# Performance work log

Measured on AMD Instinct MI355X. Metric: run time of the kernel, lower is better.

## Reference

```python
import jax, jax.numpy as jnp
import numpy as np

K = 4          # neighbors
R = 2          # step_ratio
OUT = 64       # output_size

def knn_idx(x, k):
    # x: (B, C, N) -> indices of k nearest neighbors (incl. self): (B, N, k)
    xx = jnp.sum(x * x, axis=1)                       # (B, N)
    inner = jnp.einsum('bcn,bcm->bnm', x, x)          # (B, N, N)
    neg_dist = 2.0 * inner - xx[:, :, None] - xx[:, None, :]
    _, idx = jax.lax.top_k(neg_dist, k)               # largest neg_dist = nearest
    return idx

def setup_inputs() -> dict:
    key = jax.random.key(0)
    ks = jax.random.split(key, 7)
    B, C, N = 16, 64, 2048
    s = 0.05
    return {
        'x':  jax.random.normal(ks[0], (B, C, N), jnp.float32),
        'w1': jax.random.normal(ks[1], (OUT, 2 * C), jnp.float32) * s,
        'b1': jax.random.normal(ks[2], (OUT,), jnp.float32) * s,
        'w2': jax.random.normal(ks[3], (OUT * R, 2 * C + OUT), jnp.float32) * s,
        'b2': jax.random.normal(ks[4], (OUT * R,), jnp.float32) * s,
        'w3': jax.random.normal(ks[5], (OUT, OUT), jnp.float32) * s,
        'b3': jax.random.normal(ks[6], (OUT,), jnp.float32) * s,
    }

def reference(x, w1, b1, w2, b2, w3, b3):
    B, C, N = x.shape
    idx = knn_idx(x, K)                                # (B, N, K)
    xt = jnp.transpose(x, (0, 2, 1))                   # (B, N, C)
    neighbors = xt[jnp.arange(B)[:, None, None], idx]  # (B, N, K, C)
    center = jnp.broadcast_to(xt[:, :, None, :], neighbors.shape)
    feat = jnp.concatenate([center, neighbors], axis=-1)   # (B, N, K, 2C), minus_center=False
    # get_graph_feature returns (B, 2C, N, K); module permutes to (B, 2C, K, N)
    f = jnp.transpose(feat, (0, 3, 2, 1))              # (B, 2C, K, N)
    e1 = jnp.einsum('oc,bckn->bokn', w1, f) + b1[None, :, None, None]
    e = jax.nn.relu(jnp.concatenate([e1, f], axis=1))  # (B, 2C+OUT, K, N)
    e2 = jax.nn.relu(jnp.einsum('oc,bckn->bokn', w2, e) + b2[None, :, None, None])  # (B, OUT*R, K, N)
    # permute(0,2,3,1) -> (B,K,N,OUT*R), view -> (B,K,N*R,OUT), permute -> (B,OUT,K,N*R)
    e2 = jnp.transpose(e2, (0, 2, 3, 1)).reshape(B, K, N * R, OUT)
    e2 = jnp.transpose(e2, (0, 3, 1, 2))               # (B, OUT, K, N*R)
    e3 = jnp.einsum('oc,bckn->bokn', w3, e2) + b3[None, :, None, None]
    return jnp.max(e3, axis=2)                          # (B, OUT, N*R)
```

## Files before the change

### kernel.cpp

```cpp
#include <hip/hip_runtime.h>
#include <hip/hip_bf16.h>

#define BB 16
#define CC 64
#define NN 2048
#define KK 4
#define NPART 4
#define JPER (NN / NPART)
#define NCAND 32
#define RSTRIDE 80

typedef unsigned short u16;
typedef unsigned int u32;
typedef __attribute__((ext_vector_type(4))) float f32x4;
typedef __attribute__((ext_vector_type(16))) float f32x16;
typedef __attribute__((ext_vector_type(8))) short short8;

__device__ __forceinline__ float bf2f(u16 u) {
    unsigned int x = ((unsigned int)u) << 16;
    float f;
    __builtin_memcpy(&f, &x, 4);
    return f;
}
__device__ __forceinline__ u16 f2bf(float f) {
    __hip_bfloat16 h = __float2bfloat16(f);
    u16 u;
    __builtin_memcpy(&u, &h, 2);
    return u;
}
__device__ __forceinline__ unsigned int pk2(float a, float b) {
    return (unsigned int)f2bf(a) | ((unsigned int)f2bf(b) << 16);
}
__device__ __forceinline__ u32 umx(u32 a, u32 b) { return a > b ? a : b; }
__device__ __forceinline__ u32 umn(u32 a, u32 b) { return a < b ? a : b; }

__global__ __launch_bounds__(256) void k_prep(const float* __restrict__ x,
                                              float* __restrict__ xt,
                                              double* __restrict__ xx64,
                                              u16* __restrict__ xpk,
                                              const float* __restrict__ w1,
                                              const float* __restrict__ w2,
                                              const float* __restrict__ w3,
                                              u16* __restrict__ wb1,
                                              u16* __restrict__ wb2,
                                              u16* __restrict__ wb3) {
    int b = blockIdx.y;
    int n = blockIdx.x * 256 + threadIdx.x;

    {
        int t = (blockIdx.y * gridDim.x + blockIdx.x) * 256 + threadIdx.x;
        int stride = gridDim.x * gridDim.y * 256;
        for (int idx = t; idx < 64 * 128; idx += stride) {
            int o = idx >> 7, k = idx & 127;
            int cb = o >> 4, lr = o & 15, ks = k >> 5, g = (k >> 3) & 3, e = k & 7;
            wb1[((cb * 4 + ks) * 64 + g * 16 + lr) * 8 + e] = f2bf(w1[idx]);
        }
        for (int idx = t; idx < 128 * 192; idx += stride) {
            int o = idx / 192, k = idx - o * 192;
            int cb = o >> 4, lr = o & 15, ks = k >> 5, g = (k >> 3) & 3, e = k & 7;
            wb2[((cb * 6 + ks) * 64 + g * 16 + lr) * 8 + e] = f2bf(w2[idx]);
        }
        for (int idx = t; idx < 64 * 64; idx += stride) {
            int o = idx >> 6, k = idx & 63;
            int cb = o >> 4, lr = o & 15, ks = k >> 5, g = (k >> 3) & 3, e = k & 7;
            wb3[((cb * 2 + ks) * 64 + g * 16 + lr) * 8 + e] = f2bf(w3[idx]);
        }
    }

    const float* xb = x + (size_t)b * CC * NN;
    float v[CC];
    float s = 0.f;
    double s64 = 0.0;
#pragma unroll
    for (int c = 0; c < CC; c++) {
        v[c] = xb[(size_t)c * NN + n];
        s = fmaf(v[c], v[c], s);
        s64 += (double)v[c] * (double)v[c];
    }
    float4* dst = (float4*)(xt + ((size_t)b * NN + n) * CC);
#pragma unroll
    for (int q = 0; q < 16; q++) {
        dst[q] = make_float4(v[4 * q], v[4 * q + 1], v[4 * q + 2], v[4 * q + 3]);
    }
    xx64[b * NN + n] = s64;
    u16* dp = xpk + ((size_t)b * NN + n) * RSTRIDE;
#pragma unroll
    for (int q = 0; q < 8; q++) {
        uint4 u;
        u.x = pk2(v[8 * q], v[8 * q + 1]);
        u.y = pk2(v[8 * q + 2], v[8 * q + 3]);
        u.z = pk2(v[8 * q + 4], v[8 * q + 5]);
        u.w = pk2(v[8 * q + 6], v[8 * q + 7]);
        *(uint4*)(dp + q * 8) = u;
    }
    u16 hi = f2bf(s);
    u16 lo = f2bf(s - bf2f(hi));
    uint4 u8;
    u8.x = (unsigned int)hi | ((unsigned int)lo << 16);
    u8.y = 0x00003F80u;
    u8.z = 0; u8.w = 0;
    *(uint4*)(dp + 64) = u8;
    uint4 z = {0, 0, 0, 0};
    *(uint4*)(dp + 72) = z;
}

__global__ __launch_bounds__(256) void k_knn3(const u16* __restrict__ xpk,
                                              u16* __restrict__ cand) {
    int tid = threadIdx.x;
    int lin = blockIdx.x;
    int swz = (lin & 7) * 128 + (lin >> 3);
    int ib = swz & 15;
    int part = (swz >> 4) & 3;
    int b = swz >> 6;
    int i0 = ib * 128;
    int j00 = part * JPER;

    __shared__ u16 Bb[2 * 2 * 10 * 32 * 8];

    int w = tid >> 6, l = tid & 63;
    int lc = l & 31, lh = l >> 5;
    int hb4 = lh * 4;

    short8 ifrag[5];
    {
        const u16* ip = xpk + ((size_t)b * NN + i0 + w * 32 + lc) * RSTRIDE + lh * 8;
#pragma unroll
        for (int ks = 0; ks < 4; ks++) ifrag[ks] = *(const short8*)(ip + ks * 16);
        short8 f4 = {0, 0, 0, 0, 0, 0, 0, 0};
        if (lh == 0) {
            f4[0] = (short)0xBF00;
            f4[1] = (short)0xBF00;
            f4[2] = (short)0x4300;
        }
        ifrag[4] = f4;
    }

    u32 v0 = 0, v1 = 0, v2 = 0, v3 = 0;

#define CE(a, b) { u32 mx_ = umx(a, b); b = umn(a, b); a = mx_; }

#define STAGE(rr, bf)                                                              \
    {                                                                              \
        int jb = j00 + (rr) * 64;                                                  \
        for (int g = tid; g < 640; g += 256) {                                     \
            int rw = g / 10, c = g - rw * 10;                                      \
            uint4 u = *(const uint4*)(xpk + ((size_t)b * NN + jb + rw) * RSTRIDE + \
                                      c * 8);                                      \
            int sub = rw >> 5, r32 = rw & 31;                                      \
            *(uint4*)((char*)Bb + (bf) * 10240 + sub * 5120 + c * 512 +            \
                      ((r32 ^ (c & 7)) * 16)) = u;                                 \
        }                                                                          \
    }

    STAGE(0, 0);

    for (int r = 0; r < JPER / 64; r++) {
        __syncthreads();
        if (r + 1 < JPER / 64) STAGE(r + 1, (r + 1) & 1);

        const char* bufp = (const char*)Bb + (r & 1) * 10240;
        f32x16 acc0, acc1;
#pragma unroll
        for (int e = 0; e < 16; e++) {
            acc0[e] = 0.f;
            acc1[e] = 0.f;
        }
#pragma unroll
        for (int ks = 0; ks < 5; ks++) {
            int c = ks * 2 + lh;
            int boff = c * 512 + ((lc ^ (c & 7)) * 16);
            short8 a0 = *(const short8*)(bufp + boff);
            short8 a1 = *(const short8*)(bufp + 5120 + boff);
            acc0 = __builtin_amdgcn_mfma_f32_32x32x16_bf16(a0, ifrag[ks], acc0, 0, 0, 0);
            acc1 = __builtin_amdgcn_mfma_f32_32x32x16_bf16(a1, ifrag[ks], acc1, 0, 0, 0);
        }
#pragma unroll
        for (int sub = 0; sub < 2; sub++) {
            const f32x16& acc = sub ? acc1 : acc0;
            int jlb = r * 64 + sub * 32 + hb4;
            u32 kk[16];
#pragma unroll
            for (int rg = 0; rg < 16; rg++) {
                u32 u;
                float f = acc[rg];
                __builtin_memcpy(&u, &f, 4);
                int coff = (rg & 3) + 8 * (rg >> 2);
                kk[rg] = (u & ~0x1FFu) | (u32)(jlb + coff);
            }
#pragma unroll
            for (int q = 0; q < 4; q++) {
                int p = q * 4;
                CE(kk[p + 0], kk[p + 2]); CE(kk[p + 1], kk[p + 3]);
                CE(kk[p + 0], kk[p + 1]); CE(kk[p + 2], kk[p + 3]);
                CE(kk[p + 1], kk[p + 2]);
            }
            kk[0] = umx(kk[0], kk[7]); kk[1] = umx(kk[1], kk[6]);
            kk[2] = umx(kk[2], kk[5]); kk[3] = umx(kk[3], kk[4]);
            CE(kk[0], kk[2]); CE(kk[1], kk[3]); CE(kk[0], kk[1]); CE(kk[2], kk[3]);
            kk[8] = umx(kk[8], kk[15]); kk[9] = umx(kk[9], kk[14]);
            kk[10] = umx(kk[10], kk[13]); kk[11] = umx(kk[11], kk[12]);
            CE(kk[8], kk[10]); CE(kk[9], kk[11]); CE(kk[8], kk[9]); CE(kk[10], kk[11]);
            kk[0] = umx(kk[0], kk[11]); kk[1] = umx(kk[1], kk[10]);
            kk[2] = umx(kk[2], kk[9]); kk[3] = umx(kk[3], kk[8]);
            CE(kk[0], kk[2]); CE(kk[1], kk[3]); CE(kk[0], kk[1]); CE(kk[2], kk[3]);
            v0 = umx(v0, kk[3]); v1 = umx(v1, kk[2]);
            v2 = umx(v2, kk[1]); v3 = umx(v3, kk[0]);
            CE(v0, v2); CE(v1, v3); CE(v0, v1); CE(v2, v3);
        }
    }
#undef STAGE
#undef CE

    size_t cb = ((size_t)b * NN + i0 + w * 32 + lc) * NCAND + part * 8 + lh * 4;
    cand[cb + 0] = (u16)(j00 + (v0 & 0x1FF));
    cand[cb + 1] = (u16)(j00 + (v1 & 0x1FF));
    cand[cb + 2] = (u16)(j00 + (v2 & 0x1FF));
    cand[cb + 3] = (u16)(j00 + (v3 & 0x1FF));
}

__global__ __launch_bounds__(256) void k_knn_merge(const float* __restrict__ xt,
                                                   const double* __restrict__ xx64,
                                                   const u16* __restrict__ cand,
                                                   int* __restrict__ nidx) {
    __shared__ double sv[16 * 33];
    __shared__ double sxx[16 * 33];
    __shared__ u16 jc[16 * 33];

    int tid = threadIdx.x;
    int g = tid >> 4;
    int q = tid & 15;
    int nwg8 = (int)(gridDim.x >> 3);
    int swz = (blockIdx.x & 7) * nwg8 + (blockIdx.x >> 3);
    size_t gp0 = (size_t)swz * 16;
    size_t bbase = (gp0 >> 11) << 11;

    for (int idx = tid; idx < 16 * 32; idx += 256) {
        int p = idx >> 5, c = idx & 31;
        u16 j = cand[(gp0 + p) * NCAND + c];
        jc[p * 33 + c] = j;
        sxx[p * 33 + c] = xx64[bbase + j];
    }
    __syncthreads();

    float4 a = ((const float4*)(xt + (gp0 + g) * CC))[q];

    float4 bv[NCAND];
#pragma unroll
    for (int c = 0; c < NCAND; c++) {
        bv[c] = ((const float4*)(xt + (bbase + jc[g * 33 + c]) * CC))[q];
    }

#pragma unroll
    for (int c0 = 0; c0 < NCAND; c0 += 4) {
        double d0 = (double)a.x * bv[c0 + 0].x + (double)a.y * bv[c0 + 0].y +
                    (double)a.z * bv[c0 + 0].z + (double)a.w * bv[c0 + 0].w;
        double d1 = (double)a.x * bv[c0 + 1].x + (double)a.y * bv[c0 + 1].y +
                    (double)a.z * bv[c0 + 1].z + (double)a.w * bv[c0 + 1].w;
        double d2 = (double)a.x * bv[c0 + 2].x + (double)a.y * bv[c0 + 2].y +
                    (double)a.z * bv[c0 + 2].z + (double)a.w * bv[c0 + 2].w;
        double d3 = (double)a.x * bv[c0 + 3].x + (double)a.y * bv[c0 + 3].y +
                    (double)a.z * bv[c0 + 3].z + (double)a.w * bv[c0 + 3].w;
        d0 += __shfl_xor(d0, 8); d1 += __shfl_xor(d1, 8);
        d2 += __shfl_xor(d2, 8); d3 += __shfl_xor(d3, 8);
        d0 += __shfl_xor(d0, 4); d1 += __shfl_xor(d1, 4);
        d2 += __shfl_xor(d2, 4); d3 += __shfl_xor(d3, 4);
        d0 += __shfl_xor(d0, 2); d1 += __shfl_xor(d1, 2);
        d2 += __shfl_xor(d2, 2); d3 += __shfl_xor(d3, 2);
        d0 += __shfl_xor(d0, 1); d1 += __shfl_xor(d1, 1);
        d2 += __shfl_xor(d2, 1); d3 += __shfl_xor(d3, 1);
        if (q == 0) {
            sv[g * 33 + c0 + 0] = 2.0 * d0 - sxx[g * 33 + c0 + 0];
            sv[g * 33 + c0 + 1] = 2.0 * d1 - sxx[g * 33 + c0 + 1];
            sv[g * 33 + c0 + 2] = 2.0 * d2 - sxx[g * 33 + c0 + 2];
            sv[g * 33 + c0 + 3] = 2.0 * d3 - sxx[g * 33 + c0 + 3];
        }
    }
    __syncthreads();

    if (tid < 16) {
        int p = tid;
        double v4[4];
        int id4[4];
#pragma unroll
        for (int s = 0; s < 4; s++) {
            v4[s] = -1e300;
            id4[s] = 0x7fffffff;
        }
        for (int cc = 0; cc < NCAND; cc++) {
            double cv = sv[p * 33 + cc];
            int ci = jc[p * 33 + cc];
#pragma unroll
            for (int s = 0; s < 4; s++) {
                bool take = (cv > v4[s]) || (cv == v4[s] && ci < id4[s]);
                double nv = take ? cv : v4[s];
                int ni = take ? ci : id4[s];
                double ov = take ? v4[s] : cv;
                int oi = take ? id4[s] : ci;
                v4[s] = nv;
                id4[s] = ni;
                cv = ov;
                ci = oi;
            }
        }
        size_t gp2 = gp0 + p;
#pragma unroll
        for (int s = 0; s < 4; s++) nidx[gp2 * 4 + s] = id4[s];
    }
}

__global__ __launch_bounds__(256) void k_mlp(const u16* __restrict__ xpk,
                                             const int* __restrict__ nidx,
                                             const u16* __restrict__ wb1,
                                             const u16* __restrict__ wb2,
                                             const u16* __restrict__ wb3,
                                             const float* __restrict__ b1,
                                             const float* __restrict__ b2,
                                             const float* __restrict__ b3,
                                             float* __restrict__ out) {
    int nch = blockIdx.x;
    int b = blockIdx.y;
    int n0 = nch * 16;
    int tid = threadIdx.x;

    __shared__ u16 Fb[64 * 128];
    __shared__ u16 E1b[64 * 64];
    __shared__ u16 E2b[64 * 128];
    __shared__ float Ob[64 * 36];
    __shared__ int ji[64];

    if (tid < 64) ji[tid] = nidx[((size_t)b * NN + n0) * KK + tid];
    __syncthreads();

    for (int g = tid; g < 64 * 16; g += 256) {
        int it = g >> 4, q = g & 15;
        int half = q >> 3, cq = q & 7;
        int srcn = half ? ji[it] : (n0 + (it >> 2));
        uint4 u = *(const uint4*)(xpk + ((size_t)b * NN + srcn) * RSTRIDE + cq * 8);
        int byte = (it * 256 + half * 128 + cq * 16) ^ ((it & 7) << 4);
        *(uint4*)((char*)Fb + byte) = u;
    }
    __syncthreads();

    int w = tid >> 6, l = tid & 63;
    int lr = l & 15, lg = l >> 4;

    {
        f32x4 acc[4];
#pragma unroll
        for (int g = 0; g < 4; g++) acc[g] = (f32x4){0.f, 0.f, 0.f, 0.f};
#pragma unroll
        for (int ks = 0; ks < 4; ks++) {
            short8 bw = *(const short8*)(wb1 + ((size_t)(w * 4 + ks) * 64 + l) * 8);
#pragma unroll
            for (int g = 0; g < 4; g++) {
                int arow = g * 16 + lr;
                int off = (arow * 256 + ks * 64 + lg * 16) ^ ((arow & 7) << 4);
                short8 a = *(const short8*)((const char*)Fb + off);
                acc[g] = __builtin_amdgcn_mfma_f32_16x16x32_bf16(a, bw, acc[g], 0, 0, 0);
            }
        }
        float bias = b1[w * 16 + lr];
#pragma unroll
        for (int g = 0; g < 4; g++) {
#pragma unroll
            for (int q = 0; q < 4; q++) {
                int item = g * 16 + lg * 4 + q;
                float vv = fmaxf(acc[g][q] + bias, 0.f);
                int byte = (item * 128 + (w * 16 + lr) * 2) ^ ((item & 7) << 4);
                *(u16*)((char*)E1b + byte) = f2bf(vv);
            }
        }
    }
    __syncthreads();

    {
        f32x4 acc[4][2];
#pragma unroll
        for (int g = 0; g < 4; g++)
#pragma unroll
            for (int c2 = 0; c2 < 2; c2++) acc[g][c2] = (f32x4){0.f, 0.f, 0.f, 0.f};
#pragma unroll
        for (int ks = 0; ks < 6; ks++) {
            short8 bw0 = *(const short8*)(wb2 + ((size_t)((w * 2) * 6 + ks) * 64 + l) * 8);
            short8 bw1 = *(const short8*)(wb2 + ((size_t)((w * 2 + 1) * 6 + ks) * 64 + l) * 8);
#pragma unroll
            for (int g = 0; g < 4; g++) {
                int arow = g * 16 + lr;
                int aswz = (arow & 7) << 4;
                short8 a;
                if (ks < 2) {
                    int off = (arow * 128 + ks * 64 + lg * 16) ^ aswz;
                    a = *(const short8*)((const char*)E1b + off);
                } else {
                    int off = (arow * 256 + (ks - 2) * 64 + lg * 16) ^ aswz;
                    uint4 u = *(const uint4*)((const char*)Fb + off);
                    unsigned int m;
                    m = ((u.x >> 15) & 0x10001u) * 0xFFFFu; u.x &= ~m;
                    m = ((u.y >> 15) & 0x10001u) * 0xFFFFu; u.y &= ~m;
                    m = ((u.z >> 15) & 0x10001u) * 0xFFFFu; u.z &= ~m;
                    m = ((u.w >> 15) & 0x10001u) * 0xFFFFu; u.w &= ~m;
                    __builtin_memcpy(&a, &u, 16);
                }
                acc[g][0] = __builtin_amdgcn_mfma_f32_16x16x32_bf16(a, bw0, acc[g][0], 0, 0, 0);
                acc[g][1] = __builtin_amdgcn_mfma_f32_16x16x32_bf16(a, bw1, acc[g][1], 0, 0, 0);
            }
        }
#pragma unroll
        for (int c2 = 0; c2 < 2; c2++) {
            float bias = b2[(w * 2 + c2) * 16 + lr];
#pragma unroll
            for (int g = 0; g < 4; g++) {
#pragma unroll
                for (int q = 0; q < 4; q++) {
                    int item = g * 16 + lg * 4 + q;
                    float vv = fmaxf(acc[g][c2][q] + bias, 0.f);
                    int byte = (item * 256 + ((w * 2 + c2) * 16 + lr) * 2) ^ ((item & 7) << 4);
                    *(u16*)((char*)E2b + byte) = f2bf(vv);
                }
            }
        }
    }
    __syncthreads();

    {
        f32x4 acc[4][2];
#pragma unroll
        for (int g = 0; g < 4; g++)
#pragma unroll
            for (int r = 0; r < 2; r++) acc[g][r] = (f32x4){0.f, 0.f, 0.f, 0.f};
#pragma unroll
        for (int ks = 0; ks < 2; ks++) {
            short8 bw = *(const short8*)(wb3 + ((size_t)(w * 2 + ks) * 64 + l) * 8);
#pragma unroll
            for (int g = 0; g < 4; g++) {
                int arow = g * 16 + lr;
                int aswz = (arow & 7) << 4;
#pragma unroll
                for (int r = 0; r < 2; r++) {
                    int off = (arow * 256 + r * 128 + ks * 64 + lg * 16) ^ aswz;
                    short8 a = *(const short8*)((const char*)E2b + off);
                    acc[g][r] = __builtin_amdgcn_mfma_f32_16x16x32_bf16(a, bw, acc[g][r], 0, 0, 0);
                }
            }
        }
        float bias = b3[w * 16 + lr];
        int o = w * 16 + lr;
#pragma unroll
        for (int g = 0; g < 4; g++) {
            int nl = g * 4 + lg;
#pragma unroll
            for (int r = 0; r < 2; r++) {
                float m = fmaxf(fmaxf(acc[g][r][0], acc[g][r][1]),
                                fmaxf(acc[g][r][2], acc[g][r][3])) + bias;
                Ob[o * 36 + nl * 2 + r] = m;
            }
        }
    }
    __syncthreads();

    {
        int o = tid >> 2, q = tid & 3;
        float4 v0 = *(const float4*)&Ob[o * 36 + q * 8];
        float4 v1 = *(const float4*)&Ob[o * 36 + q * 8 + 4];
        float* dst = out + ((size_t)(b * 64 + o)) * 4096 + n0 * 2 + q * 8;
        ((float4*)dst)[0] = v0;
        ((float4*)dst)[1] = v1;
    }
}

extern "C" void kernel_launch(void* const* d_in, const int* in_sizes, int n_in,
                              void* d_out, int out_size, void* d_ws, size_t ws_size,
                              hipStream_t stream) {
    const float* x = (const float*)d_in[0];
    const float* w1 = (const float*)d_in[1];
    const float* b1 = (const float*)d_in[2];
    const float* w2 = (const float*)d_in[3];
    const float* b2 = (const float*)d_in[4];
    const float* w3 = (const float*)d_in[5];
    const float* b3 = (const float*)d_in[6];
    float* out = (float*)d_out;

    float* xt = (float*)d_ws;
    u16* xpk = (u16*)(xt + (size_t)BB * NN * CC);
    double* xx64 = (double*)(xpk + (size_t)BB * NN * RSTRIDE);
    int* nidx = (int*)(xx64 + (size_t)BB * NN);
    u16* cand = (u16*)(nidx + (size_t)BB * NN * KK);
    u16* wb1 = cand + (size_t)BB * NN * NCAND;
    u16* wb2 = wb1 + 64 * 128;
    u16* wb3 = wb2 + 128 * 192;

    k_prep<<<dim3(NN / 256, BB), 256, 0, stream>>>(x, xt, xx64, xpk,
                                                   w1, w2, w3, wb1, wb2, wb3);
    k_knn3<<<dim3(NN / 128 * NPART * BB), 256, 0, stream>>>(xpk, cand);
    k_knn_merge<<<dim3(BB * NN / 16), 256, 0, stream>>>(xt, xx64, cand, nidx);
    k_mlp<<<dim3(NN / 16, BB), 256, 0, stream>>>(xpk, nidx, wb1, wb2, wb3, b1, b2, b3, out);
}
```

Before: 107.4 us.

## Fuse knn, merge and MLP kernels into one persistent kernel with grid barriers

Replaces three separate launches (candidate kNN, merge, MLP) with a single persistent kernel of 768 blocks. The blocks loop over work units for each phase and separate the phases with a spin-on-atomic grid barrier. The barrier counter is reset in the prep kernel. This removes inter-kernel launch gaps and tail effects. In exchange it relies on all 768 blocks being co-resident (launch_bounds 256,3 with about 50KB of shared memory), otherwise the barrier can deadlock or time out. It also adds the cost of atomic spinning.

```diff
diff --git a/kernel.cpp b/kernel.cpp
--- a/kernel.cpp
+++ b/kernel.cpp
@@ -9,6 +9,7 @@
 #define JPER (NN / NPART)
 #define NCAND 32
 #define RSTRIDE 80
+#define GRID_F 768
 
 typedef unsigned short u16;
 typedef unsigned int u32;
@@ -43,7 +44,9 @@
                                               const float* __restrict__ w3,
                                               u16* __restrict__ wb1,
                                               u16* __restrict__ wb2,
-                                              u16* __restrict__ wb3) {
+                                              u16* __restrict__ wb3,
+                                              u32* __restrict__ bar) {
+    if (blockIdx.x == 0 && blockIdx.y == 0 && threadIdx.x < 2) bar[threadIdx.x] = 0;
     int b = blockIdx.y;
     int n = blockIdx.x * 256 + threadIdx.x;
 
@@ -104,367 +107,386 @@
     *(uint4*)(dp + 72) = z;
 }
 
-__global__ __launch_bounds__(256) void k_knn3(const u16* __restrict__ xpk,
-                                              u16* __restrict__ cand) {
+__device__ __forceinline__ void grid_bar(u32* cnt, u32 target) {
+    __syncthreads();
+    if (threadIdx.x == 0) {
+        __threadfence();
+        atomicAdd(cnt, 1u);
+        int it = 0;
+        while (atomicAdd(cnt, 0u) < target && it < 100000000) it++;
+        __threadfence();
+    }
+    __syncthreads();
+}
+
+__global__ __launch_bounds__(256, 3) void k_fused(const float* __restrict__ xt,
+                                                  const double* __restrict__ xx64,
+                                                  const u16* __restrict__ xpk,
+                                                  u16* __restrict__ cand,
+                                                  int* __restrict__ nidx,
+                                                  const u16* __restrict__ wb1,
+                                                  const u16* __restrict__ wb2,
+                                                  const u16* __restrict__ wb3,
+                                                  const float* __restrict__ b1,
+                                                  const float* __restrict__ b2,
+                                                  const float* __restrict__ b3,
+                                                  float* __restrict__ out,
+                                                  u32* __restrict__ bar) {
+    __shared__ __align__(16) char smem[50432];
     int tid = threadIdx.x;
     int lin = blockIdx.x;
-    int swz = (lin & 7) * 128 + (lin >> 3);
-    int ib = swz & 15;
-    int part = (swz >> 4) & 3;
-    int b = swz >> 6;
-    int i0 = ib * 128;
-    int j00 = part * JPER;
-
-    __shared__ u16 Bb[2 * 2 * 10 * 32 * 8];
-
-    int w = tid >> 6, l = tid & 63;
-    int lc = l & 31, lh = l >> 5;
-    int hb4 = lh * 4;
-
-    short8 ifrag[5];
-    {
-        const u16* ip = xpk + ((size_t)b * NN + i0 + w * 32 + lc) * RSTRIDE + lh * 8;
-#pragma unroll
-        for (int ks = 0; ks < 4; ks++) ifrag[ks] = *(const short8*)(ip + ks * 16);
-        short8 f4 = {0, 0, 0, 0, 0, 0, 0, 0};
-        if (lh == 0) {
-            f4[0] = (short)0xBF00;
-            f4[1] = (short)0xBF00;
-            f4[2] = (short)0x4300;
-        }
-        ifrag[4] = f4;
-    }
-
-    u32 v0 = 0, v1 = 0, v2 = 0, v3 = 0;
+
+    for (int u = lin; u < 1024; u += GRID_F) {
+        __syncthreads();
+        int swz = (u & 7) * 128 + (u >> 3);
+        int ib = swz & 15;
+        int part = (swz >> 4) & 3;
+        int b = swz >> 6;
+        int i0 = ib * 128;
+        int j00 = part * JPER;
+        u16* Bb = (u16*)smem;
+
+        int w = tid >> 6, l = tid & 63;
+        int lc = l & 31, lh = l >> 5;
+        int hb4 = lh * 4;
+
+        short8 ifrag[5];
+        {
+            const u16* ip = xpk + ((size_t)b * NN + i0 + w * 32 + lc) * RSTRIDE + lh * 8;
+#pragma unroll
+            for (int ks = 0; ks < 4; ks++) ifrag[ks] = *(const short8*)(ip + ks * 16);
+            short8 f4 = {0, 0, 0, 0, 0, 0, 0, 0};
+            if (lh == 0) {
+                f4[0] = (short)0xBF00;
+                f4[1] = (short)0xBF00;
+                f4[2] = (short)0x4300;
+            }
+            ifrag[4] = f4;
+        }
+
+        u32 v0 = 0, v1 = 0, v2 = 0, v3 = 0;
 
 #define CE(a, b) { u32 mx_ = umx(a, b); b = umn(a, b); a = mx_; }
-
 #define STAGE(rr, bf)                                                              \
     {                                                                              \
         int jb = j00 + (rr) * 64;                                                  \
         for (int g = tid; g < 640; g += 256) {                                     \
             int rw = g / 10, c = g - rw * 10;                                      \
-            uint4 u = *(const uint4*)(xpk + ((size_t)b * NN + jb + rw) * RSTRIDE + \
+            uint4 uu = *(const uint4*)(xpk + ((size_t)b * NN + jb + rw) * RSTRIDE +\
                                       c * 8);                                      \
             int sub = rw >> 5, r32 = rw & 31;                                      \
             *(uint4*)((char*)Bb + (bf) * 10240 + sub * 5120 + c * 512 +            \
-                      ((r32 ^ (c & 7)) * 16)) = u;                                 \
+                      ((r32 ^ (c & 7)) * 16)) = uu;                                \
         }                                                                          \
     }
 
-    STAGE(0, 0);
-
-    for (int r = 0; r < JPER / 64; r++) {
-        __syncthreads();
-        if (r + 1 < JPER / 64) STAGE(r + 1, (r + 1) & 1);
-
-        const char* bufp = (const char*)Bb + (r & 1) * 10240;
-        f32x16 acc0, acc1;
-#pragma unroll
-        for (int e = 0; e < 16; e++) {
-            acc0[e] = 0.f;
-            acc1[e] = 0.f;
-        }
-#pragma unroll
-        for (int ks = 0; ks < 5; ks++) {
-            int c = ks * 2 + lh;
-            int boff = c * 512 + ((lc ^ (c & 7)) * 16);
-            short8 a0 = *(const short8*)(bufp + boff);
-            short8 a1 = *(const short8*)(bufp + 5120 + boff);
-            acc0 = __builtin_amdgcn_mfma_f32_32x32x16_bf16(a0, ifrag[ks], acc0, 0, 0, 0);
-            acc1 = __builtin_amdgcn_mfma_f32_32x32x16_bf16(a1, ifrag[ks], acc1, 0, 0, 0);
-        }
-#pragma unroll
-        for (int sub = 0; sub < 2; sub++) {
-            const f32x16& acc = sub ? acc1 : acc0;
-            int jlb = r * 64 + sub * 32 + hb4;
-            u32 kk[16];
-#pragma unroll
-            for (int rg = 0; rg < 16; rg++) {
-                u32 u;
-                float f = acc[rg];
-                __builtin_memcpy(&u, &f, 4);
-                int coff = (rg & 3) + 8 * (rg >> 2);
-                kk[rg] = (u & ~0x1FFu) | (u32)(jlb + coff);
-            }
-#pragma unroll
-            for (int q = 0; q < 4; q++) {
-                int p = q * 4;
-                CE(kk[p + 0], kk[p + 2]); CE(kk[p + 1], kk[p + 3]);
-                CE(kk[p + 0], kk[p + 1]); CE(kk[p + 2], kk[p + 3]);
-                CE(kk[p + 1], kk[p + 2]);
-            }
-            kk[0] = umx(kk[0], kk[7]); kk[1] = umx(kk[1], kk[6]);
-            kk[2] = umx(kk[2], kk[5]); kk[3] = umx(kk[3], kk[4]);
-            CE(kk[0], kk[2]); CE(kk[1], kk[3]); CE(kk[0], kk[1]); CE(kk[2], kk[3]);
-            kk[8] = umx(kk[8], kk[15]); kk[9] = umx(kk[9], kk[14]);
-            kk[10] = umx(kk[10], kk[13]); kk[11] = umx(kk[11], kk[12]);
-            CE(kk[8], kk[10]); CE(kk[9], kk[11]); CE(kk[8], kk[9]); CE(kk[10], kk[11]);
-            kk[0] = umx(kk[0], kk[11]); kk[1] = umx(kk[1], kk[10]);
-            kk[2] = umx(kk[2], kk[9]); kk[3] = umx(kk[3], kk[8]);
-            CE(kk[0], kk[2]); CE(kk[1], kk[3]); CE(kk[0], kk[1]); CE(kk[2], kk[3]);
-            v0 = umx(v0, kk[3]); v1 = umx(v1, kk[2]);
-            v2 = umx(v2, kk[1]); v3 = umx(v3, kk[0]);
-            CE(v0, v2); CE(v1, v3); CE(v0, v1); CE(v2, v3);
-        }
-    }
+        STAGE(0, 0);
+
+        for (int r = 0; r < JPER / 64; r++) {
+            __syncthreads();
+            if (r + 1 < JPER / 64) STAGE(r + 1, (r + 1) & 1);
+
+            const char* bufp = (const char*)Bb + (r & 1) * 10240;
+            f32x16 acc0, acc1;
+#pragma unroll
+            for (int e = 0; e < 16; e++) {
+                acc0[e] = 0.f;
+                acc1[e] = 0.f;
+            }
+#pragma unroll
+            for (int ks = 0; ks < 5; ks++) {
+                int c = ks * 2 + lh;
+                int boff = c * 512 + ((lc ^ (c & 7)) * 16);
+                short8 a0 = *(const short8*)(bufp + boff);
+                short8 a1 = *(const short8*)(bufp + 5120 + boff);
+                acc0 = __builtin_amdgcn_mfma_f32_32x32x16_bf16(a0, ifrag[ks], acc0, 0, 0, 0);
+                acc1 = __builtin_amdgcn_mfma_f32_32x32x16_bf16(a1, ifrag[ks], acc1, 0, 0, 0);
+            }
+#pragma unroll
+            for (int sub = 0; sub < 2; sub++) {
+                const f32x16& acc = sub ? acc1 : acc0;
+                int jlb = r * 64 + sub * 32 + hb4;
+                u32 kk[16];
+#pragma unroll
+                for (int rg = 0; rg < 16; rg++) {
+                    u32 uu;
+                    float f = acc[rg];
+                    __builtin_memcpy(&uu, &f, 4);
+                    int coff = (rg & 3) + 8 * (rg >> 2);
+                    kk[rg] = (uu & ~0x1FFu) | (u32)(jlb + coff);
+                }
+#pragma unroll
+                for (int q = 0; q < 4; q++) {
+                    int p = q * 4;
+                    CE(kk[p + 0], kk[p + 2]); CE(kk[p + 1], kk[p + 3]);
+                    CE(kk[p + 0], kk[p + 1]); CE(kk[p + 2], kk[p + 3]);
+                    CE(kk[p + 1], kk[p + 2]);
+                }
+                kk[0] = umx(kk[0], kk[7]); kk[1] = umx(kk[1], kk[6]);
+                kk[2] = umx(kk[2], kk[5]); kk[3] = umx(kk[3], kk[4]);
+                CE(kk[0], kk[2]); CE(kk[1], kk[3]); CE(kk[0], kk[1]); CE(kk[2], kk[3]);
+                kk[8] = umx(kk[8], kk[15]); kk[9] = umx(kk[9], kk[14]);
+                kk[10] = umx(kk[10], kk[13]); kk[11] = umx(kk[11], kk[12]);
+                CE(kk[8], kk[10]); CE(kk[9], kk[11]); CE(kk[8], kk[9]); CE(kk[10], kk[11]);
+                kk[0] = umx(kk[0], kk[11]); kk[1] = umx(kk[1], kk[10]);
+                kk[2] = umx(kk[2], kk[9]); kk[3] = umx(kk[3], kk[8]);
+                CE(kk[0], kk[2]); CE(kk[1], kk[3]); CE(kk[0], kk[1]); CE(kk[2], kk[3]);
+                v0 = umx(v0, kk[3]); v1 = umx(v1, kk[2]);
+                v2 = umx(v2, kk[1]); v3 = umx(v3, kk[0]);
+                CE(v0, v2); CE(v1, v3); CE(v0, v1); CE(v2, v3);
+            }
+        }
 #undef STAGE
 #undef CE
 
-    size_t cb = ((size_t)b * NN + i0 + w * 32 + lc) * NCAND + part * 8 + lh * 4;
-    cand[cb + 0] = (u16)(j00 + (v0 & 0x1FF));
-    cand[cb + 1] = (u16)(j00 + (v1 & 0x1FF));
-    cand[cb + 2] = (u16)(j00 + (v2 & 0x1FF));
-    cand[cb + 3] = (u16)(j00 + (v3 & 0x1FF));
-}
-
-__global__ __launch_bounds__(256) void k_knn_merge(const float* __restrict__ xt,
-                                                   const double* __restrict__ xx64,
-                                                   const u16* __restrict__ cand,
-                                                   int* __restrict__ nidx) {
-    __shared__ double sv[16 * 33];
-    __shared__ double sxx[16 * 33];
-    __shared__ u16 jc[16 * 33];
-
-    int tid = threadIdx.x;
-    int g = tid >> 4;
-    int q = tid & 15;
-    int nwg8 = (int)(gridDim.x >> 3);
-    int swz = (blockIdx.x & 7) * nwg8 + (blockIdx.x >> 3);
-    size_t gp0 = (size_t)swz * 16;
-    size_t bbase = (gp0 >> 11) << 11;
-
-    for (int idx = tid; idx < 16 * 32; idx += 256) {
-        int p = idx >> 5, c = idx & 31;
-        u16 j = cand[(gp0 + p) * NCAND + c];
-        jc[p * 33 + c] = j;
-        sxx[p * 33 + c] = xx64[bbase + j];
-    }
-    __syncthreads();
-
-    float4 a = ((const float4*)(xt + (gp0 + g) * CC))[q];
-
-    float4 bv[NCAND];
-#pragma unroll
-    for (int c = 0; c < NCAND; c++) {
-        bv[c] = ((const float4*)(xt + (bbase + jc[g * 33 + c]) * CC))[q];
-    }
-
-#pragma unroll
-    for (int c0 = 0; c0 < NCAND; c0 += 4) {
-        double d0 = (double)a.x * bv[c0 + 0].x + (double)a.y * bv[c0 + 0].y +
-                    (double)a.z * bv[c0 + 0].z + (double)a.w * bv[c0 + 0].w;
-        double d1 = (double)a.x * bv[c0 + 1].x + (double)a.y * bv[c0 + 1].y +
-                    (double)a.z * bv[c0 + 1].z + (double)a.w * bv[c0 + 1].w;
-        double d2 = (double)a.x * bv[c0 + 2].x + (double)a.y * bv[c0 + 2].y +
-                    (double)a.z * bv[c0 + 2].z + (double)a.w * bv[c0 + 2].w;
-        double d3 = (double)a.x * bv[c0 + 3].x + (double)a.y * bv[c0 + 3].y +
-                    (double)a.z * bv[c0 + 3].z + (double)a.w * bv[c0 + 3].w;
-        d0 += __shfl_xor(d0, 8); d1 += __shfl_xor(d1, 8);
-        d2 += __shfl_xor(d2, 8); d3 += __shfl_xor(d3, 8);
-        d0 += __shfl_xor(d0, 4); d1 += __shfl_xor(d1, 4);
-        d2 += __shfl_xor(d2, 4); d3 += __shfl_xor(d3, 4);
-        d0 += __shfl_xor(d0, 2); d1 += __shfl_xor(d1, 2);
-        d2 += __shfl_xor(d2, 2); d3 += __shfl_xor(d3, 2);
-        d0 += __shfl_xor(d0, 1); d1 += __shfl_xor(d1, 1);
-        d2 += __shfl_xor(d2, 1); d3 += __shfl_xor(d3, 1);
-        if (q == 0) {
-            sv[g * 33 + c0 + 0] = 2.0 * d0 - sxx[g * 33 + c0 + 0];
-            sv[g * 33 + c0 + 1] = 2.0 * d1 - sxx[g * 33 + c0 + 1];
-            sv[g * 33 + c0 + 2] = 2.0 * d2 - sxx[g * 33 + c0 + 2];
-            sv[g * 33 + c0 + 3] = 2.0 * d3 - sxx[g * 33 + c0 + 3];
-        }
-    }
-    __syncthreads();
-
-    if (tid < 16) {
-        int p = tid;
-        double v4[4];
-        int id4[4];
-#pragma unroll
-        for (int s = 0; s < 4; s++) {
-            v4[s] = -1e300;
-            id4[s] = 0x7fffffff;
-        }
-        for (int cc = 0; cc < NCAND; cc++) {
-            double cv = sv[p * 33 + cc];
-            int ci = jc[p * 33 + cc];
+        size_t cb = ((size_t)b * NN + i0 + w * 32 + lc) * NCAND + part * 8 + lh * 4;
+        cand[cb + 0] = (u16)(j00 + (v0 & 0x1FF));
+        cand[cb + 1] = (u16)(j00 + (v1 & 0x1FF));
+        cand[cb + 2] = (u16)(j00 + (v2 & 0x1FF));
+        cand[cb + 3] = (u16)(j00 + (v3 & 0x1FF));
+    }
+
+    grid_bar(&bar[0], GRID_F);
+
+    for (int u = lin; u < 2048; u += GRID_F) {
+        __syncthreads();
+        double* sv = (double*)smem;
+        double* sxx = (double*)(smem + 4224);
+        u16* jc = (u16*)(smem + 8448);
+
+        int g = tid >> 4;
+        int q = tid & 15;
+        int swz = (u & 7) * 256 + (u >> 3);
+        size_t gp0 = (size_t)swz * 16;
+        size_t bbase = (gp0 >> 11) << 11;
+
+        for (int idx = tid; idx < 16 * 32; idx += 256) {
+            int p = idx >> 5, c = idx & 31;
+            u16 j = cand[(gp0 + p) * NCAND + c];
+            jc[p * 33 + c] = j;
+            sxx[p * 33 + c] = xx64[bbase + j];
+        }
+        __syncthreads();
+
+        float4 a = ((const float4*)(xt + (gp0 + g) * CC))[q];
+
+        float4 bv[NCAND];
+#pragma unroll
+        for (int c = 0; c < NCAND; c++) {
+            bv[c] = ((const float4*)(xt + (bbase + jc[g * 33 + c]) * CC))[q];
+        }
+
+#pragma unroll
+        for (int c0 = 0; c0 < NCAND; c0 += 4) {
+            double d0 = (double)a.x * bv[c0 + 0].x + (double)a.y * bv[c0 + 0].y +
+                        (double)a.z * bv[c0 + 0].z + (double)a.w * bv[c0 + 0].w;
+            double d1 = (double)a.x * bv[c0 + 1].x + (double)a.y * bv[c0 + 1].y +
+                        (double)a.z * bv[c0 + 1].z + (double)a.w * bv[c0 + 1].w;
+            double d2 = (double)a.x * bv[c0 + 2].x + (double)a.y * bv[c0 + 2].y +
+                        (double)a.z * bv[c0 + 2].z + (double)a.w * bv[c0 + 2].w;
+            double d3 = (double)a.x * bv[c0 + 3].x + (double)a.y * bv[c0 + 3].y +
+                        (double)a.z * bv[c0 + 3].z + (double)a.w * bv[c0 + 3].w;
+            d0 += __shfl_xor(d0, 8); d1 += __shfl_xor(d1, 8);
+            d2 += __shfl_xor(d2, 8); d3 += __shfl_xor(d3, 8);
+            d0 += __shfl_xor(d0, 4); d1 += __shfl_xor(d1, 4);
+            d2 += __shfl_xor(d2, 4); d3 += __shfl_xor(d3, 4);
+            d0 += __shfl_xor(d0, 2); d1 += __shfl_xor(d1, 2);
+            d2 += __shfl_xor(d2, 2); d3 += __shfl_xor(d3, 2);
+            d0 += __shfl_xor(d0, 1); d1 += __shfl_xor(d1, 1);
+            d2 += __shfl_xor(d2, 1); d3 += __shfl_xor(d3, 1);
+            if (q == 0) {
+                sv[g * 33 + c0 + 0] = 2.0 * d0 - sxx[g * 33 + c0 + 0];
+                sv[g * 33 + c0 + 1] = 2.0 * d1 - sxx[g * 33 + c0 + 1];
+                sv[g * 33 + c0 + 2] = 2.0 * d2 - sxx[g * 33 + c0 + 2];
+                sv[g * 33 + c0 + 3] = 2.0 * d3 - sxx[g * 33 + c0 + 3];
+            }
+        }
+        __syncthreads();
+
+        if (tid < 16) {
+            int p = tid;
+            double v4[4];
+            int id4[4];
 #pragma unroll
             for (int s = 0; s < 4; s++) {
-                bool take = (cv > v4[s]) || (cv == v4[s] && ci < id4[s]);
-                double nv = take ? cv : v4[s];
-                int ni = take ? ci : id4[s];
-                double ov = take ? v4[s] : cv;
-                int oi = take ? id4[s] : ci;
-                v4[s] = nv;
-                id4[s] = ni;
-                cv = ov;
-                ci = oi;
-            }
-        }
-        size_t gp2 = gp0 + p;
-#pragma unroll
-        for (int s = 0; s < 4; s++) nidx[gp2 * 4 + s] = id4[s];
-    }
-}
-
-__global__ __launch_bounds__(256) void k_mlp(const u16* __restrict__ xpk,
-                                             const int* __restrict__ nidx,
-                                             const u16* __restrict__ wb1,
-                                             const u16* __restrict__ wb2,
-                                             const u16* __restrict__ wb3,
-                                             const float* __restrict__ b1,
-                                             const float* __restrict__ b2,
-                                             const float* __restrict__ b3,
-                                             float* __restrict__ out) {
-    int nch = blockIdx.x;
-    int b = blockIdx.y;
-    int n0 = nch * 16;
-    int tid = threadIdx.x;
-
-    __shared__ u16 Fb[64 * 128];
-    __shared__ u16 E1b[64 * 64];
-    __shared__ u16 E2b[64 * 128];
-    __shared__ float Ob[64 * 36];
-    __shared__ int ji[64];
-
-    if (tid < 64) ji[tid] = nidx[((size_t)b * NN + n0) * KK + tid];
-    __syncthreads();
-
-    for (int g = tid; g < 64 * 16; g += 256) {
-        int it = g >> 4, q = g & 15;
-        int half = q >> 3, cq = q & 7;
-        int srcn = half ? ji[it] : (n0 + (it >> 2));
-        uint4 u = *(const uint4*)(xpk + ((size_t)b * NN + srcn) * RSTRIDE + cq * 8);
-        int byte = (it * 256 + half * 128 + cq * 16) ^ ((it & 7) << 4);
-        *(uint4*)((char*)Fb + byte) = u;
-    }
-    __syncthreads();
-
-    int w = tid >> 6, l = tid & 63;
-    int lr = l & 15, lg = l >> 4;
-
-    {
-        f32x4 acc[4];
-#pragma unroll
-        for (int g = 0; g < 4; g++) acc[g] = (f32x4){0.f, 0.f, 0.f, 0.f};
-#pragma unroll
-        for (int ks = 0; ks < 4; ks++) {
-            short8 bw = *(const short8*)(wb1 + ((size_t)(w * 4 + ks) * 64 + l) * 8);
-#pragma unroll
-            for (int g = 0; g < 4; g++) {
-                int arow = g * 16 + lr;
-                int off = (arow * 256 + ks * 64 + lg * 16) ^ ((arow & 7) << 4);
-                short8 a = *(const short8*)((const char*)Fb + off);
-                acc[g] = __builtin_amdgcn_mfma_f32_16x16x32_bf16(a, bw, acc[g], 0, 0, 0);
-            }
-        }
-        float bias = b1[w * 16 + lr];
-#pragma unroll
-        for (int g = 0; g < 4; g++) {
-#pragma unroll
-            for (int q = 0; q < 4; q++) {
-                int item = g * 16 + lg * 4 + q;
-                float vv = fmaxf(acc[g][q] + bias, 0.f);
-                int byte = (item * 128 + (w * 16 + lr) * 2) ^ ((item & 7) << 4);
-                *(u16*)((char*)E1b + byte) = f2bf(vv);
-            }
-        }
-    }
-    __syncthreads();
-
-    {
-        f32x4 acc[4][2];
-#pragma unroll
-        for (int g = 0; g < 4; g++)
-#pragma unroll
-            for (int c2 = 0; c2 < 2; c2++) acc[g][c2] = (f32x4){0.f, 0.f, 0.f, 0.f};
-#pragma unroll
-        for (int ks = 0; ks < 6; ks++) {
-            short8 bw0 = *(const short8*)(wb2 + ((size_t)((w * 2) * 6 + ks) * 64 + l) * 8);
-            short8 bw1 = *(const short8*)(wb2 + ((size_t)((w * 2 + 1) * 6 + ks) * 64 + l) * 8);
-#pragma unroll
-            for (int g = 0; g < 4; g++) {
-                int arow = g * 16 + lr;
-                int aswz = (arow & 7) << 4;
-                short8 a;
-                if (ks < 2) {
-                    int off = (arow * 128 + ks * 64 + lg * 16) ^ aswz;
-                    a = *(const short8*)((const char*)E1b + off);
-                } else {
-                    int off = (arow * 256 + (ks - 2) * 64 + lg * 16) ^ aswz;
-                    uint4 u = *(const uint4*)((const char*)Fb + off);
-                    unsigned int m;
-                    m = ((u.x >> 15) & 0x10001u) * 0xFFFFu; u.x &= ~m;
-                    m = ((u.y >> 15) & 0x10001u) * 0xFFFFu; u.y &= ~m;
-                    m = ((u.z >> 15) & 0x10001u) * 0xFFFFu; u.z &= ~m;
-                    m = ((u.w >> 15) & 0x10001u) * 0xFFFFu; u.w &= ~m;
-                    __builtin_memcpy(&a, &u, 16);
-                }
-                acc[g][0] = __builtin_amdgcn_mfma_f32_16x16x32_bf16(a, bw0, acc[g][0], 0, 0, 0);
-                acc[g][1] = __builtin_amdgcn_mfma_f32_16x16x32_bf16(a, bw1, acc[g][1], 0, 0, 0);
-            }
-        }
-#pragma unroll
-        for (int c2 = 0; c2 < 2; c2++) {
-            float bias = b2[(w * 2 + c2) * 16 + lr];
+                v4[s] = -1e300;
+                id4[s] = 0x7fffffff;
+            }
+            for (int cc = 0; cc < NCAND; cc++) {
+                double cv = sv[p * 33 + cc];
+                int ci = jc[p * 33 + cc];
+#pragma unroll
+                for (int s = 0; s < 4; s++) {
+                    bool take = (cv > v4[s]) || (cv == v4[s] && ci < id4[s]);
+                    double nv = take ? cv : v4[s];
+                    int ni = take ? ci : id4[s];
+                    double ov = take ? v4[s] : cv;
+                    int oi = take ? id4[s] : ci;
+                    v4[s] = nv;
+                    id4[s] = ni;
+                    cv = ov;
+                    ci = oi;
+                }
+            }
+            size_t gp2 = gp0 + p;
+#pragma unroll
+            for (int s = 0; s < 4; s++) nidx[gp2 * 4 + s] = id4[s];
+        }
+    }
+
+    grid_bar(&bar[1], GRID_F);
+
+    for (int u = lin; u < 2048; u += GRID_F) {
+        __syncthreads();
+        int swz = (u & 7) * 256 + (u >> 3);
+        int b = swz >> 7;
+        int nch = swz & 127;
+        int n0 = nch * 16;
+
+        u16* Fb = (u16*)smem;
+        u16* E1b = (u16*)(smem + 16384);
+        u16* E2b = (u16*)(smem + 24576);
+        float* Ob = (float*)(smem + 40960);
+        int* ji = (int*)(smem + 50176);
+
+        if (tid < 64) ji[tid] = nidx[((size_t)b * NN + n0) * KK + tid];
+        __syncthreads();
+
+        for (int g = tid; g < 64 * 16; g += 256) {
+            int it = g >> 4, q = g & 15;
+            int half = q >> 3, cq = q & 7;
+            int srcn = half ? ji[it] : (n0 + (it >> 2));
+            uint4 uu = *(const uint4*)(xpk + ((size_t)b * NN + srcn) * RSTRIDE + cq * 8);
+            int byte = (it * 256 + half * 128 + cq * 16) ^ ((it & 7) << 4);
+            *(uint4*)((char*)Fb + byte) = uu;
+        }
+        __syncthreads();
+
+        int w = tid >> 6, l = tid & 63;
+        int lr = l & 15, lg = l >> 4;
+
+        {
+            f32x4 acc[4];
+#pragma unroll
+            for (int g = 0; g < 4; g++) acc[g] = (f32x4){0.f, 0.f, 0.f, 0.f};
+#pragma unroll
+            for (int ks = 0; ks < 4; ks++) {
+                short8 bw = *(const short8*)(wb1 + ((size_t)(w * 4 + ks) * 64 + l) * 8);
+#pragma unroll
+                for (int g = 0; g < 4; g++) {
+                    int arow = g * 16 + lr;
+                    int off = (arow * 256 + ks * 64 + lg * 16) ^ ((arow & 7) << 4);
+                    short8 a = *(const short8*)((const char*)Fb + off);
+                    acc[g] = __builtin_amdgcn_mfma_f32_16x16x32_bf16(a, bw, acc[g], 0, 0, 0);
+                }
+            }
+            float bias = b1[w * 16 + lr];
 #pragma unroll
             for (int g = 0; g < 4; g++) {
 #pragma unroll
                 for (int q = 0; q < 4; q++) {
                     int item = g * 16 + lg * 4 + q;
-                    float vv = fmaxf(acc[g][c2][q] + bias, 0.f);
-                    int byte = (item * 256 + ((w * 2 + c2) * 16 + lr) * 2) ^ ((item & 7) << 4);
-                    *(u16*)((char*)E2b + byte) = f2bf(vv);
-                }
-            }
-        }
-    }
-    __syncthreads();
-
-    {
-        f32x4 acc[4][2];
-#pragma unroll
-        for (int g = 0; g < 4; g++)
-#pragma unroll
-            for (int r = 0; r < 2; r++) acc[g][r] = (f32x4){0.f, 0.f, 0.f, 0.f};
-#pragma unroll
-        for (int ks = 0; ks < 2; ks++) {
-            short8 bw = *(const short8*)(wb3 + ((size_t)(w * 2 + ks) * 64 + l) * 8);
+                    float vv = fmaxf(acc[g][q] + bias, 0.f);
+                    int byte = (item * 128 + (w * 16 + lr) * 2) ^ ((item & 7) << 4);
+                    *(u16*)((char*)E1b + byte) = f2bf(vv);
+                }
+            }
+        }
+        __syncthreads();
+
+        {
+            f32x4 acc[4][2];
+#pragma unroll
+            for (int g = 0; g < 4; g++)
+#pragma unroll
+                for (int c2 = 0; c2 < 2; c2++) acc[g][c2] = (f32x4){0.f, 0.f, 0.f, 0.f};
+#pragma unroll
+            for (int ks = 0; ks < 6; ks++) {
+                short8 bw0 = *(const short8*)(wb2 + ((size_t)((w * 2) * 6 + ks) * 64 + l) * 8);
+                short8 bw1 = *(const short8*)(wb2 + ((size_t)((w * 2 + 1) * 6 + ks) * 64 + l) * 8);
+#pragma unroll
+                for (int g = 0; g < 4; g++) {
+                    int arow = g * 16 + lr;
+                    int aswz = (arow & 7) << 4;
+                    short8 a;
+                    if (ks < 2) {
+                        int off = (arow * 128 + ks * 64 + lg * 16) ^ aswz;
+                        a = *(const short8*)((const char*)E1b + off);
+                    } else {
+                        int off = (arow * 256 + (ks - 2) * 64 + lg * 16) ^ aswz;
+                        uint4 uu = *(const uint4*)((const char*)Fb + off);
+                        unsigned int m;
+                        m = ((uu.x >> 15) & 0x10001u) * 0xFFFFu; uu.x &= ~m;
+                        m = ((uu.y >> 15) & 0x10001u) * 0xFFFFu; uu.y &= ~m;
+                        m = ((uu.z >> 15) & 0x10001u) * 0xFFFFu; uu.z &= ~m;
+                        m = ((uu.w >> 15) & 0x10001u) * 0xFFFFu; uu.w &= ~m;
+                        __builtin_memcpy(&a, &uu, 16);
+                    }
+                    acc[g][0] = __builtin_amdgcn_mfma_f32_16x16x32_bf16(a, bw0, acc[g][0], 0, 0, 0);
+                    acc[g][1] = __builtin_amdgcn_mfma_f32_16x16x32_bf16(a, bw1, acc[g][1], 0, 0, 0);
+                }
+            }
+#pragma unroll
+            for (int c2 = 0; c2 < 2; c2++) {
+                float bias = b2[(w * 2 + c2) * 16 + lr];
+#pragma unroll
+                for (int g = 0; g < 4; g++) {
+#pragma unroll
+                    for (int q = 0; q < 4; q++) {
+                        int item = g * 16 + lg * 4 + q;
+                        float vv = fmaxf(acc[g][c2][q] + bias, 0.f);
+                        int byte = (item * 256 + ((w * 2 + c2) * 16 + lr) * 2) ^ ((item & 7) << 4);
+                        *(u16*)((char*)E2b + byte) = f2bf(vv);
+                    }
+                }
+            }
+        }
+        __syncthreads();
+
+        {
+            f32x4 acc[4][2];
+#pragma unroll
+            for (int g = 0; g < 4; g++)
+#pragma unroll
+                for (int r = 0; r < 2; r++) acc[g][r] = (f32x4){0.f, 0.f, 0.f, 0.f};
+#pragma unroll
+            for (int ks = 0; ks < 2; ks++) {
+                short8 bw = *(const short8*)(wb3 + ((size_t)(w * 2 + ks) * 64 + l) * 8);
+#pragma unroll
+                for (int g = 0; g < 4; g++) {
+                    int arow = g * 16 + lr;
+                    int aswz = (arow & 7) << 4;
+#pragma unroll
+                    for (int r = 0; r < 2; r++) {
+                        int off = (arow * 256 + r * 128 + ks * 64 + lg * 16) ^ aswz;
+                        short8 a = *(const short8*)((const char*)E2b + off);
+                        acc[g][r] = __builtin_amdgcn_mfma_f32_16x16x32_bf16(a, bw, acc[g][r], 0, 0, 0);
+                    }
+                }
+            }
+            float bias = b3[w * 16 + lr];
+            int o = w * 16 + lr;
 #pragma unroll
             for (int g = 0; g < 4; g++) {
-                int arow = g * 16 + lr;
-                int aswz = (arow & 7) << 4;
+                int nl = g * 4 + lg;
 #pragma unroll
                 for (int r = 0; r < 2; r++) {
-                    int off = (arow * 256 + r * 128 + ks * 64 + lg * 16) ^ aswz;
-                    short8 a = *(const short8*)((const char*)E2b + off);
-                    acc[g][r] = __builtin_amdgcn_mfma_f32_16x16x32_bf16(a, bw, acc[g][r], 0, 0, 0);
-                }
-            }
-        }
-        float bias = b3[w * 16 + lr];
-        int o = w * 16 + lr;
-#pragma unroll
-        for (int g = 0; g < 4; g++) {
-            int nl = g * 4 + lg;
-#pragma unroll
-            for (int r = 0; r < 2; r++) {
-                float m = fmaxf(fmaxf(acc[g][r][0], acc[g][r][1]),
-                                fmaxf(acc[g][r][2], acc[g][r][3])) + bias;
-                Ob[o * 36 + nl * 2 + r] = m;
-            }
-        }
-    }
-    __syncthreads();
-
-    {
-        int o = tid >> 2, q = tid & 3;
-        float4 v0 = *(const float4*)&Ob[o * 36 + q * 8];
-        float4 v1 = *(const float4*)&Ob[o * 36 + q * 8 + 4];
-        float* dst = out + ((size_t)(b * 64 + o)) * 4096 + n0 * 2 + q * 8;
-        ((float4*)dst)[0] = v0;
-        ((float4*)dst)[1] = v1;
+                    float m = fmaxf(fmaxf(acc[g][r][0], acc[g][r][1]),
+                                    fmaxf(acc[g][r][2], acc[g][r][3])) + bias;
+                    Ob[o * 36 + nl * 2 + r] = m;
+                }
+            }
+        }
+        __syncthreads();
+
+        {
+            int o = tid >> 2, q = tid & 3;
+            float4 v0 = *(const float4*)&Ob[o * 36 + q * 8];
+            float4 v1 = *(const float4*)&Ob[o * 36 + q * 8 + 4];
+            float* dst = out + ((size_t)(b * 64 + o)) * 4096 + n0 * 2 + q * 8;
+            ((float4*)dst)[0] = v0;
+            ((float4*)dst)[1] = v1;
+        }
     }
 }
 
@@ -488,10 +510,10 @@
     u16* wb1 = cand + (size_t)BB * NN * NCAND;
     u16* wb2 = wb1 + 64 * 128;
     u16* wb3 = wb2 + 128 * 192;
+    u32* bar = (u32*)(wb3 + 64 * 64);
 
     k_prep<<<dim3(NN / 256, BB), 256, 0, stream>>>(x, xt, xx64, xpk,
-                                                   w1, w2, w3, wb1, wb2, wb3);
-    k_knn3<<<dim3(NN / 128 * NPART * BB), 256, 0, stream>>>(xpk, cand);
-    k_knn_merge<<<dim3(BB * NN / 16), 256, 0, stream>>>(xt, xx64, cand, nidx);
-    k_mlp<<<dim3(NN / 16, BB), 256, 0, stream>>>(xpk, nidx, wb1, wb2, wb3, b1, b2, b3, out);
-}
+                                                   w1, w2, w3, wb1, wb2, wb3, bar);
+    k_fused<<<dim3(GRID_F), 256, 0, stream>>>(xt, xx64, xpk, cand, nidx,
+                                              wb1, wb2, wb3, b1, b2, b3, out, bar);
+}
```

New measurement: 308.6 us. 187% more time.
